# Kernel tuning notes

Measured on AMD Instinct MI355X. Metric: run time of the kernel, lower is better.

The kernel has to match this reference:

```python
import jax, jax.numpy as jnp
import numpy as np

VOCAB, DIM, HID, OUT = 400000, 300, 32, 2
BATCH, SEQ = 16384, 50

def setup_inputs() -> dict:
    key = jax.random.key(0)
    k_tok, k_emb, k_vw, k_vb, k_ww, k_wb = jax.random.split(key, 6)
    tokens = jax.random.randint(k_tok, (BATCH, SEQ), 0, VOCAB, dtype=jnp.int32)
    emb = jax.random.normal(k_emb, (VOCAB, DIM), dtype=jnp.float32) * 0.02
    emb = emb.at[0].set(0.0)  # padding_idx=0 row conventionally zero
    V_w = jax.random.normal(k_vw, (HID, DIM), dtype=jnp.float32) * (1.0 / np.sqrt(DIM))
    V_b = jnp.zeros((HID,), dtype=jnp.float32)
    W_w = jax.random.normal(k_ww, (OUT, HID), dtype=jnp.float32) * (1.0 / np.sqrt(HID))
    W_b = jnp.zeros((OUT,), dtype=jnp.float32)
    return {"tokens": tokens, "emb": emb, "V_w": V_w, "V_b": V_b, "W_w": W_w, "W_b": W_b}

def reference(tokens, emb, V_w, V_b, W_w, W_b):
    # gather [B,S,D] then mean-pool over words -> [B,D] (DAN average)
    pooled = jnp.mean(emb[tokens], axis=1)
    h = jax.nn.relu(pooled @ V_w.T + V_b)          # [B,HID]
    logits = h @ W_w.T + W_b                        # [B,OUT]
    # original module uses LogSoftmax(dim=0): normalize over the batch axis
    return jax.nn.log_softmax(logits, axis=0)
```

## Files before the change

### kernel.cpp

```cpp
#include <hip/hip_runtime.h>

#define VOCAB 400000
#define DIM   300
#define HID   32
#define NOUT  2
#define BATCH 16384
#define SEQ   50

__global__ __launch_bounds__(256) void dan_main(
    const int*   __restrict__ tokens,
    const float* __restrict__ emb,
    const float* __restrict__ Vw,
    const float* __restrict__ Vb,
    const float* __restrict__ Ww,
    const float* __restrict__ Wb,
    float*       __restrict__ logits)
{
    const int wave = threadIdx.x >> 6;
    const int lane = threadIdx.x & 63;
    const int row  = blockIdx.x * 4 + wave;
    if (row >= BATCH) return;

    const int* toks = tokens + row * SEQ;

    const bool has1 = (lane < (DIM / 4 - 64));

    float4 acc0 = make_float4(0.f, 0.f, 0.f, 0.f);
    float4 acc1 = make_float4(0.f, 0.f, 0.f, 0.f);

    for (int s = 0; s < SEQ; ++s) {
        const int t = toks[s];
        const float4* e = (const float4*)(emb + (size_t)t * DIM);
        float4 v0 = e[lane];
        acc0.x += v0.x; acc0.y += v0.y; acc0.z += v0.z; acc0.w += v0.w;
        if (has1) {
            float4 v1 = e[64 + lane];
            acc1.x += v1.x; acc1.y += v1.y; acc1.z += v1.z; acc1.w += v1.w;
        }
    }
    const float inv = 1.0f / (float)SEQ;
    acc0.x *= inv; acc0.y *= inv; acc0.z *= inv; acc0.w *= inv;
    acc1.x *= inv; acc1.y *= inv; acc1.z *= inv; acc1.w *= inv;

    float hp[HID];
    #pragma unroll
    for (int k = 0; k < HID; ++k) {
        const float4* vr = (const float4*)(Vw + k * DIM);
        float4 w0 = vr[lane];
        float p = acc0.x * w0.x + acc0.y * w0.y + acc0.z * w0.z + acc0.w * w0.w;
        if (has1) {
            float4 w1 = vr[64 + lane];
            p += acc1.x * w1.x + acc1.y * w1.y + acc1.z * w1.z + acc1.w * w1.w;
        }
        hp[k] = p;
    }

    #pragma unroll
    for (int m = 1; m < 64; m <<= 1) {
        #pragma unroll
        for (int k = 0; k < HID; ++k)
            hp[k] += __shfl_xor(hp[k], m, 64);
    }

    float l0 = Wb[0], l1 = Wb[1];
    #pragma unroll
    for (int k = 0; k < HID; ++k) {
        float h = hp[k] + Vb[k];
        h = h > 0.f ? h : 0.f;
        l0 += h * Ww[k];
        l1 += h * Ww[HID + k];
    }
    if (lane == 0) {
        logits[row * 2 + 0] = l0;
        logits[row * 2 + 1] = l1;
    }
}

__global__ __launch_bounds__(1024) void dan_reduce(
    const float* __restrict__ logits, float* __restrict__ c)
{
    __shared__ float r0[1024];
    __shared__ float r1[1024];
    const int tid = threadIdx.x;

    float m0 = -INFINITY, m1 = -INFINITY;
    for (int b = tid; b < BATCH; b += 1024) {
        m0 = fmaxf(m0, logits[b * 2 + 0]);
        m1 = fmaxf(m1, logits[b * 2 + 1]);
    }
    r0[tid] = m0; r1[tid] = m1;
    __syncthreads();
    for (int s = 512; s > 0; s >>= 1) {
        if (tid < s) {
            r0[tid] = fmaxf(r0[tid], r0[tid + s]);
            r1[tid] = fmaxf(r1[tid], r1[tid + s]);
        }
        __syncthreads();
    }
    m0 = r0[0]; m1 = r1[0];
    __syncthreads();

    float s0 = 0.f, s1 = 0.f;
    for (int b = tid; b < BATCH; b += 1024) {
        s0 += __expf(logits[b * 2 + 0] - m0);
        s1 += __expf(logits[b * 2 + 1] - m1);
    }
    r0[tid] = s0; r1[tid] = s1;
    __syncthreads();
    for (int s = 512; s > 0; s >>= 1) {
        if (tid < s) {
            r0[tid] += r0[tid + s];
            r1[tid] += r1[tid + s];
        }
        __syncthreads();
    }
    if (tid == 0) {
        c[0] = m0 + __logf(r0[0]);
        c[1] = m1 + __logf(r1[0]);
    }
}

__global__ __launch_bounds__(256) void dan_final(
    const float* __restrict__ logits, const float* __restrict__ c,
    float* __restrict__ out)
{
    const int idx = blockIdx.x * blockDim.x + threadIdx.x;
    if (idx < BATCH * NOUT)
        out[idx] = logits[idx] - c[idx & 1];
}

extern "C" void kernel_launch(void* const* d_in, const int* in_sizes, int n_in,
                              void* d_out, int out_size, void* d_ws, size_t ws_size,
                              hipStream_t stream) {
    const int*   tokens = (const int*)  d_in[0];
    const float* emb    = (const float*)d_in[1];
    const float* Vw     = (const float*)d_in[2];
    const float* Vb     = (const float*)d_in[3];
    const float* Ww     = (const float*)d_in[4];
    const float* Wb     = (const float*)d_in[5];
    float* out    = (float*)d_out;
    float* logits = (float*)d_ws;
    float* c      = logits + BATCH * NOUT;

    dan_main  <<<BATCH / 4, 256, 0, stream>>>(tokens, emb, Vw, Vb, Ww, Wb, logits);
    dan_reduce<<<1, 1024, 0, stream>>>(logits, c);
    dan_final <<<(BATCH * NOUT + 255) / 256, 256, 0, stream>>>(logits, c, out);
}
```

Before: 771.5 us.

## Batch embedding gathers with lane-loaded tokens and vectorize logit accesses

Each wave now loads its 50 tokens once, one per lane, and broadcasts them with shuffles. Embedding rows are gathered five at a time so more independent loads are in flight before accumulation, hiding gather latency in this memory-bound kernel. The logits reads and writes in the reduce and final kernels use float2 accesses, and the final kernel runs one thread per row. The cost is more live registers for the batched loads, which could reduce occupancy.

Result: slower. 831.4 us (+7.8%).

```diff
diff --git a/kernel.cpp b/kernel.cpp
--- a/kernel.cpp
+++ b/kernel.cpp
@@ -21,38 +21,59 @@
     const int row  = blockIdx.x * 4 + wave;
     if (row >= BATCH) return;
 
-    const int* toks = tokens + row * SEQ;
+    int tl = 0;
+    if (lane < SEQ) tl = tokens[row * SEQ + lane];
 
     const bool has1 = (lane < (DIM / 4 - 64));
 
-    float4 acc0 = make_float4(0.f, 0.f, 0.f, 0.f);
-    float4 acc1 = make_float4(0.f, 0.f, 0.f, 0.f);
+    float4 a0 = make_float4(0.f, 0.f, 0.f, 0.f);
+    float4 a1 = make_float4(0.f, 0.f, 0.f, 0.f);
 
-    for (int s = 0; s < SEQ; ++s) {
-        const int t = toks[s];
-        const float4* e = (const float4*)(emb + (size_t)t * DIM);
-        float4 v0 = e[lane];
-        acc0.x += v0.x; acc0.y += v0.y; acc0.z += v0.z; acc0.w += v0.w;
+    for (int s0 = 0; s0 < SEQ; s0 += 5) {
+        const float4* e[5];
+        #pragma unroll
+        for (int j = 0; j < 5; ++j) {
+            const int t = __shfl(tl, s0 + j, 64);
+            e[j] = (const float4*)(emb + (size_t)t * DIM);
+        }
+        float4 v0[5];
+        #pragma unroll
+        for (int j = 0; j < 5; ++j) v0[j] = e[j][lane];
+        float4 v1[5];
         if (has1) {
-            float4 v1 = e[64 + lane];
-            acc1.x += v1.x; acc1.y += v1.y; acc1.z += v1.z; acc1.w += v1.w;
+            #pragma unroll
+            for (int j = 0; j < 5; ++j) v1[j] = e[j][64 + lane];
+        }
+        #pragma unroll
+        for (int j = 0; j < 5; ++j) {
+            a0.x += v0[j].x; a0.y += v0[j].y; a0.z += v0[j].z; a0.w += v0[j].w;
+        }
+        if (has1) {
+            #pragma unroll
+            for (int j = 0; j < 5; ++j) {
+                a1.x += v1[j].x; a1.y += v1[j].y; a1.z += v1[j].z; a1.w += v1[j].w;
+            }
         }
     }
     const float inv = 1.0f / (float)SEQ;
-    acc0.x *= inv; acc0.y *= inv; acc0.z *= inv; acc0.w *= inv;
-    acc1.x *= inv; acc1.y *= inv; acc1.z *= inv; acc1.w *= inv;
+    a0.x *= inv; a0.y *= inv; a0.z *= inv; a0.w *= inv;
+    a1.x *= inv; a1.y *= inv; a1.z *= inv; a1.w *= inv;
 
     float hp[HID];
     #pragma unroll
-    for (int k = 0; k < HID; ++k) {
-        const float4* vr = (const float4*)(Vw + k * DIM);
-        float4 w0 = vr[lane];
-        float p = acc0.x * w0.x + acc0.y * w0.y + acc0.z * w0.z + acc0.w * w0.w;
-        if (has1) {
-            float4 w1 = vr[64 + lane];
-            p += acc1.x * w1.x + acc1.y * w1.y + acc1.z * w1.z + acc1.w * w1.w;
+    for (int half = 0; half < 2; ++half) {
+        #pragma unroll
+        for (int kk = 0; kk < 16; ++kk) {
+            const int k = half * 16 + kk;
+            const float4* vr = (const float4*)(Vw + k * DIM);
+            float4 w0 = vr[lane];
+            float p = a0.x * w0.x + a0.y * w0.y + a0.z * w0.z + a0.w * w0.w;
+            if (has1) {
+                float4 w1 = vr[64 + lane];
+                p += a1.x * w1.x + a1.y * w1.y + a1.z * w1.z + a1.w * w1.w;
+            }
+            hp[k] = p;
         }
-        hp[k] = p;
     }
 
     #pragma unroll
@@ -71,8 +92,7 @@
         l1 += h * Ww[HID + k];
     }
     if (lane == 0) {
-        logits[row * 2 + 0] = l0;
-        logits[row * 2 + 1] = l1;
+        ((float2*)logits)[row] = make_float2(l0, l1);
     }
 }
 
@@ -82,11 +102,13 @@
     __shared__ float r0[1024];
     __shared__ float r1[1024];
     const int tid = threadIdx.x;
+    const float2* lp = (const float2*)logits;
 
     float m0 = -INFINITY, m1 = -INFINITY;
     for (int b = tid; b < BATCH; b += 1024) {
-        m0 = fmaxf(m0, logits[b * 2 + 0]);
-        m1 = fmaxf(m1, logits[b * 2 + 1]);
+        float2 v = lp[b];
+        m0 = fmaxf(m0, v.x);
+        m1 = fmaxf(m1, v.y);
     }
     r0[tid] = m0; r1[tid] = m1;
     __syncthreads();
@@ -102,8 +124,9 @@
 
     float s0 = 0.f, s1 = 0.f;
     for (int b = tid; b < BATCH; b += 1024) {
-        s0 += __expf(logits[b * 2 + 0] - m0);
-        s1 += __expf(logits[b * 2 + 1] - m1);
+        float2 v = lp[b];
+        s0 += __expf(v.x - m0);
+        s1 += __expf(v.y - m1);
     }
     r0[tid] = s0; r1[tid] = s1;
     __syncthreads();
@@ -124,9 +147,11 @@
     const float* __restrict__ logits, const float* __restrict__ c,
     float* __restrict__ out)
 {
-    const int idx = blockIdx.x * blockDim.x + threadIdx.x;
-    if (idx < BATCH * NOUT)
-        out[idx] = logits[idx] - c[idx & 1];
+    const int b = blockIdx.x * blockDim.x + threadIdx.x;
+    if (b < BATCH) {
+        float2 v = ((const float2*)logits)[b];
+        ((float2*)out)[b] = make_float2(v.x - c[0], v.y - c[1]);
+    }
 }
 
 extern "C" void kernel_launch(void* const* d_in, const int* in_sizes, int n_in,
@@ -144,5 +169,5 @@
 
     dan_main  <<<BATCH / 4, 256, 0, stream>>>(tokens, emb, Vw, Vb, Ww, Wb, logits);
     dan_reduce<<<1, 1024, 0, stream>>>(logits, c);
-    dan_final <<<(BATCH * NOUT + 255) / 256, 256, 0, stream>>>(logits, c, out);
+    dan_final <<<(BATCH + 255) / 256, 256, 0, stream>>>(logits, c, out);
 }
```

## Precompute embedding-times-V projection table, then gather 32-wide projected rows

Applied to the files above, without the earlier changes.

Uses linearity of mean pooling and the linear layer to precompute P = emb @ V_w^T for the whole vocabulary in a new kernel, so the per-batch gather reads 32 floats per token instead of 300. The pre-pass streams the entire 480 MB embedding table and writes a 51 MB table each call, where the original gather touched only about 820K random rows. The reduce and final kernels are also vectorised. Whether this wins depends on full-table streaming bandwidth versus random row-gather traffic. The per-thread 32-accumulator loop with an LDS-resident 38 KB V_w may limit occupancy.

Measured after the change: 879.8 us. 14.0% more time.

```diff
diff --git a/kernel.cpp b/kernel.cpp
--- a/kernel.cpp
+++ b/kernel.cpp
@@ -7,10 +7,47 @@
 #define BATCH 16384
 #define SEQ   50
 
-__global__ __launch_bounds__(256) void dan_main(
-    const int*   __restrict__ tokens,
+__global__ __launch_bounds__(256) void dan_pre(
     const float* __restrict__ emb,
     const float* __restrict__ Vw,
+    float*       __restrict__ P)
+{
+    __shared__ float vwlds[HID * DIM];
+    for (int i = threadIdx.x; i < HID * DIM; i += 256)
+        vwlds[i] = Vw[i];
+    __syncthreads();
+
+    const int row = blockIdx.x * 256 + threadIdx.x;
+    if (row >= VOCAB) return;
+
+    const float4* erow = (const float4*)(emb + (size_t)row * DIM);
+    const float4* wt   = (const float4*)vwlds;
+
+    float acc[HID];
+    #pragma unroll
+    for (int k = 0; k < HID; ++k) acc[k] = 0.f;
+
+    for (int d4 = 0; d4 < DIM / 4; ++d4) {
+        const float4 ev = erow[d4];
+        #pragma unroll
+        for (int k = 0; k < HID; ++k) {
+            const float4 w = wt[k * (DIM / 4) + d4];
+            acc[k] = fmaf(ev.x, w.x, acc[k]);
+            acc[k] = fmaf(ev.y, w.y, acc[k]);
+            acc[k] = fmaf(ev.z, w.z, acc[k]);
+            acc[k] = fmaf(ev.w, w.w, acc[k]);
+        }
+    }
+
+    float4* prow = (float4*)(P + (size_t)row * HID);
+    #pragma unroll
+    for (int j = 0; j < HID / 4; ++j)
+        prow[j] = make_float4(acc[4*j], acc[4*j+1], acc[4*j+2], acc[4*j+3]);
+}
+
+__global__ __launch_bounds__(256) void dan_gather(
+    const int*   __restrict__ tokens,
+    const float* __restrict__ P,
     const float* __restrict__ Vb,
     const float* __restrict__ Ww,
     const float* __restrict__ Wb,
@@ -21,59 +58,32 @@
     const int row  = blockIdx.x * 4 + wave;
     if (row >= BATCH) return;
 
-    const int* toks = tokens + row * SEQ;
+    int tl = 0;
+    if (lane < SEQ) tl = tokens[row * SEQ + lane];
 
-    const bool has1 = (lane < (DIM / 4 - 64));
+    const int k    = lane & 31;
+    const int half = lane >> 5;
 
-    float4 acc0 = make_float4(0.f, 0.f, 0.f, 0.f);
-    float4 acc1 = make_float4(0.f, 0.f, 0.f, 0.f);
+    float acc = 0.f;
+    #pragma unroll
+    for (int i = 0; i < SEQ / 2; ++i) {
+        const int t = __shfl(tl, 2 * i + half, 64);
+        acc += P[(size_t)t * HID + k];
+    }
+    acc += __shfl_xor(acc, 32, 64);
 
-    for (int s = 0; s < SEQ; ++s) {
-        const int t = toks[s];
-        const float4* e = (const float4*)(emb + (size_t)t * DIM);
-        float4 v0 = e[lane];
-        acc0.x += v0.x; acc0.y += v0.y; acc0.z += v0.z; acc0.w += v0.w;
-        if (has1) {
-            float4 v1 = e[64 + lane];
-            acc1.x += v1.x; acc1.y += v1.y; acc1.z += v1.z; acc1.w += v1.w;
-        }
+    float h = acc * (1.0f / (float)SEQ) + Vb[k];
+    h = h > 0.f ? h : 0.f;
+
+    float p0 = h * Ww[k];
+    float p1 = h * Ww[HID + k];
+    #pragma unroll
+    for (int m = 16; m >= 1; m >>= 1) {
+        p0 += __shfl_xor(p0, m, 64);
+        p1 += __shfl_xor(p1, m, 64);
     }
-    const float inv = 1.0f / (float)SEQ;
-    acc0.x *= inv; acc0.y *= inv; acc0.z *= inv; acc0.w *= inv;
-    acc1.x *= inv; acc1.y *= inv; acc1.z *= inv; acc1.w *= inv;
-
-    float hp[HID];
-    #pragma unroll
-    for (int k = 0; k < HID; ++k) {
-        const float4* vr = (const float4*)(Vw + k * DIM);
-        float4 w0 = vr[lane];
-        float p = acc0.x * w0.x + acc0.y * w0.y + acc0.z * w0.z + acc0.w * w0.w;
-        if (has1) {
-            float4 w1 = vr[64 + lane];
-            p += acc1.x * w1.x + acc1.y * w1.y + acc1.z * w1.z + acc1.w * w1.w;
-        }
-        hp[k] = p;
-    }
-
-    #pragma unroll
-    for (int m = 1; m < 64; m <<= 1) {
-        #pragma unroll
-        for (int k = 0; k < HID; ++k)
-            hp[k] += __shfl_xor(hp[k], m, 64);
-    }
-
-    float l0 = Wb[0], l1 = Wb[1];
-    #pragma unroll
-    for (int k = 0; k < HID; ++k) {
-        float h = hp[k] + Vb[k];
-        h = h > 0.f ? h : 0.f;
-        l0 += h * Ww[k];
-        l1 += h * Ww[HID + k];
-    }
-    if (lane == 0) {
-        logits[row * 2 + 0] = l0;
-        logits[row * 2 + 1] = l1;
-    }
+    if (lane == 0)
+        ((float2*)logits)[row] = make_float2(p0 + Wb[0], p1 + Wb[1]);
 }
 
 __global__ __launch_bounds__(1024) void dan_reduce(
@@ -82,11 +92,13 @@
     __shared__ float r0[1024];
     __shared__ float r1[1024];
     const int tid = threadIdx.x;
+    const float4* lp = (const float4*)logits;
 
     float m0 = -INFINITY, m1 = -INFINITY;
-    for (int b = tid; b < BATCH; b += 1024) {
-        m0 = fmaxf(m0, logits[b * 2 + 0]);
-        m1 = fmaxf(m1, logits[b * 2 + 1]);
+    for (int i = tid; i < BATCH / 2; i += 1024) {
+        float4 v = lp[i];
+        m0 = fmaxf(m0, fmaxf(v.x, v.z));
+        m1 = fmaxf(m1, fmaxf(v.y, v.w));
     }
     r0[tid] = m0; r1[tid] = m1;
     __syncthreads();
@@ -101,9 +113,10 @@
     __syncthreads();
 
     float s0 = 0.f, s1 = 0.f;
-    for (int b = tid; b < BATCH; b += 1024) {
-        s0 += __expf(logits[b * 2 + 0] - m0);
-        s1 += __expf(logits[b * 2 + 1] - m1);
+    for (int i = tid; i < BATCH / 2; i += 1024) {
+        float4 v = lp[i];
+        s0 += __expf(v.x - m0) + __expf(v.z - m0);
+        s1 += __expf(v.y - m1) + __expf(v.w - m1);
     }
     r0[tid] = s0; r1[tid] = s1;
     __syncthreads();
@@ -124,9 +137,11 @@
     const float* __restrict__ logits, const float* __restrict__ c,
     float* __restrict__ out)
 {
-    const int idx = blockIdx.x * blockDim.x + threadIdx.x;
-    if (idx < BATCH * NOUT)
-        out[idx] = logits[idx] - c[idx & 1];
+    const int b = blockIdx.x * blockDim.x + threadIdx.x;
+    if (b < BATCH) {
+        float2 v = ((const float2*)logits)[b];
+        ((float2*)out)[b] = make_float2(v.x - c[0], v.y - c[1]);
+    }
 }
 
 extern "C" void kernel_launch(void* const* d_in, const int* in_sizes, int n_in,
@@ -138,11 +153,14 @@
     const float* Vb     = (const float*)d_in[3];
     const float* Ww     = (const float*)d_in[4];
     const float* Wb     = (const float*)d_in[5];
-    float* out    = (float*)d_out;
-    float* logits = (float*)d_ws;
+    float* out = (float*)d_out;
+
+    float* P      = (float*)d_ws;
+    float* logits = P + (size_t)VOCAB * HID;
     float* c      = logits + BATCH * NOUT;
 
-    dan_main  <<<BATCH / 4, 256, 0, stream>>>(tokens, emb, Vw, Vb, Ww, Wb, logits);
+    dan_pre   <<<(VOCAB + 255) / 256, 256, 0, stream>>>(emb, Vw, P);
+    dan_gather<<<BATCH / 4, 256, 0, stream>>>(tokens, P, Vb, Ww, Wb, logits);
     dan_reduce<<<1, 1024, 0, stream>>>(logits, c);
-    dan_final <<<(BATCH * NOUT + 255) / 256, 256, 0, stream>>>(logits, c, out);
+    dan_final <<<(BATCH + 255) / 256, 256, 0, stream>>>(logits, c, out);
 }
```
